# Kernel tuning notes

Hardware: AMD Instinct MI355X
Metric: run time of the kernel (lower is better)

The kernel has to match this reference:

```python
import jax, jax.numpy as jnp
import numpy as np

VOCAB, EMB, HID = 50257, 256, 512
B, S = 64, 512


def setup_inputs() -> dict:
    key = jax.random.key(0)
    ks = jax.random.split(key, 11)
    sc = 0.05
    return {
        "inputs": jax.random.randint(ks[0], (B, S), 0, VOCAB, dtype=jnp.int32),
        "emb": jax.random.normal(ks[1], (VOCAB, EMB), jnp.float32) * sc,
        "Wi": jax.random.normal(ks[2], (EMB, 4 * HID), jnp.float32) * sc,   # kernel, gate order i|f|g|o (Keras)
        "Wh": jax.random.normal(ks[3], (HID, 4 * HID), jnp.float32) * sc,   # recurrent kernel
        "b": jax.random.normal(ks[4], (4 * HID,), jnp.float32) * sc,
        "W1": jax.random.normal(ks[5], (HID, HID), jnp.float32) * sc,
        "b1": jnp.zeros((HID,), jnp.float32),
        "W2": jax.random.normal(ks[6], (HID, HID), jnp.float32) * sc,
        "b2": jnp.zeros((HID,), jnp.float32),
        "W3": jax.random.normal(ks[7], (HID, VOCAB), jnp.float32) * sc,
        "b3": jnp.zeros((VOCAB,), jnp.float32),
    }


def _lstm_final_h(x, Wi, Wh, b):
    # x: [B, S, E] -> final hidden state [B, H]
    Bsz = x.shape[0]
    H = Wh.shape[0]
    h0 = jnp.zeros((Bsz, H), x.dtype)
    c0 = jnp.zeros((Bsz, H), x.dtype)

    def step(carry, xt):
        h, c = carry
        z = xt @ Wi + h @ Wh + b              # [B, 4H]
        i, f, g, o = jnp.split(z, 4, axis=-1)  # Keras gate order: input, forget, cell, output
        i = jax.nn.sigmoid(i)
        f = jax.nn.sigmoid(f)
        g = jnp.tanh(g)
        o = jax.nn.sigmoid(o)
        c = f * c + i * g
        h = o * jnp.tanh(c)
        return (h, c), None

    (h, _), _ = jax.lax.scan(step, (h0, c0), jnp.swapaxes(x, 0, 1))  # scan over time [S, B, E]
    return h


def reference(inputs, emb, Wi, Wh, b, W1, b1, W2, b2, W3, b3):
    src_emb = emb[inputs]                      # [B, S, E] embedding lookup
    enc_hidden = _lstm_final_h(src_emb, Wi, Wh, b)  # [B, H]
    y = jnp.tanh(enc_hidden @ W1 + b1)
    y = jnp.tanh(y @ W2 + b2)
    logits = y @ W3 + b3                       # [B, vocab]
    return jax.nn.log_softmax(logits, axis=-1)
```

## Files before the change

### kernel.cpp

```cpp
#include <hip/hip_runtime.h>
#include <hip/hip_bf16.h>

#define VOCAB 50257
#define EMBD  256
#define HID   512
#define BATCH 64
#define SEQ   512

typedef short bf16x8 __attribute__((ext_vector_type(8)));
typedef float f32x4  __attribute__((ext_vector_type(4)));

__device__ inline short f2b(float f) {
    union { float f; unsigned u; } v; v.f = f;
    unsigned r = v.u + 0x7FFFu + ((v.u >> 16) & 1u);
    return (short)(r >> 16);
}
__device__ inline unsigned pack2_trunc(float lo, float hi) {
    union { float f; unsigned u; } a, b; a.f = lo; b.f = hi;
    return __builtin_amdgcn_perm(b.u, a.u, 0x07060302);
}
__device__ inline float fast_tanh(float x) {
    x = fminf(fmaxf(x, -15.f), 15.f);
    float e = __expf(2.f * x);
    return (e - 1.f) / (e + 1.f);
}
__device__ inline float fast_sig(float x) { return 1.f / (1.f + __expf(-x)); }

__device__ inline void load_x_frags(const float* __restrict__ emb, int idxv, int quad, bf16x8* Ax) {
#pragma unroll
    for (int kt = 0; kt < 8; ++kt) {
        const float* p = emb + (size_t)idxv * EMBD + kt * 32 + quad * 8;
        float4 e0 = *(const float4*)(p);
        float4 e1 = *(const float4*)(p + 4);
        union { bf16x8 v; unsigned u[4]; } f;
        f.u[0] = pack2_trunc(e0.x, e0.y);
        f.u[1] = pack2_trunc(e0.z, e0.w);
        f.u[2] = pack2_trunc(e1.x, e1.y);
        f.u[3] = pack2_trunc(e1.z, e1.w);
        Ax[kt] = f.v;
    }
}

__global__ __launch_bounds__(256, 1) void lstm_kernel(
    const int* __restrict__ idx, const float* __restrict__ emb,
    const float* __restrict__ Wi, const float* __restrict__ Wh,
    const float* __restrict__ bvec,
    unsigned long long* __restrict__ hbuf ,
    unsigned short* __restrict__ hfinal )
{
    const int wgid = blockIdx.x;
    const int grp  = wgid >> 5;
    const int jj   = wgid & 31;
    const int tid  = threadIdx.x;
    const int lane = tid & 63;
    const int w    = tid >> 6;
    const int quad = lane >> 4;
    const int l16  = lane & 15;
    const int cbase = jj * 16 + w * 4;
    const int wcol  = (l16 & 3) * HID + cbase + (l16 >> 2);
    const int arow  = grp * 16 + l16;

    __shared__ __align__(16) unsigned hstageF[2][4096];

    bf16x8 Bh[16], Bx[8];
#pragma unroll
    for (int kt = 0; kt < 16; ++kt)
#pragma unroll
        for (int i = 0; i < 8; ++i)
            Bh[kt][i] = f2b(Wh[(size_t)(kt * 32 + quad * 8 + i) * 2048 + wcol]);
#pragma unroll
    for (int kt = 0; kt < 8; ++kt)
#pragma unroll
        for (int i = 0; i < 8; ++i)
            Bx[kt][i] = f2b(Wi[(size_t)(kt * 32 + quad * 8 + i) * 2048 + wcol]);

    float bvr[4];
#pragma unroll
    for (int r = 0; r < 4; ++r) bvr[r] = bvec[r * HID + cbase + quad];

    bf16x8 Ax[8];
    load_x_frags(emb, idx[arow * SEQ], quad, Ax);

    const int scp = jj * 8 + w * 2 + (quad >> 1);
    const int su  = (scp >> 4) * 256 + ((scp >> 2) & 3) * 64 + l16 * 4 + (scp & 3);

    float cs = 0.f;

    for (int t = 0; t < SEQ; ++t) {
        const unsigned long long* rbase =
            hbuf + ((size_t)((t & 1) * 4 + grp) * 4096 + w * 1024 + lane);

        unsigned long long v[16];
        if (t > 0) {
#pragma unroll
            for (int i = 0; i < 16; ++i)
                v[i] = __hip_atomic_load(rbase + i * 64,
                                         __ATOMIC_RELAXED, __HIP_MEMORY_SCOPE_AGENT);
        }

        f32x4 a0 = {0.f, 0.f, 0.f, 0.f}, a1 = {0.f, 0.f, 0.f, 0.f};
#pragma unroll
        for (int kt = 0; kt < 8; kt += 2) {
            a0 = __builtin_amdgcn_mfma_f32_16x16x32_bf16(Bx[kt],     Ax[kt],     a0, 0, 0, 0);
            a1 = __builtin_amdgcn_mfma_f32_16x16x32_bf16(Bx[kt + 1], Ax[kt + 1], a1, 0, 0, 0);
        }

        if (t > 0) {
            const unsigned tg = (unsigned)t;
            while (true) {
                bool ok = true;
#pragma unroll
                for (int i = 0; i < 16; ++i)
                    ok = ok && ((unsigned)(v[i] >> 32) == tg);
                if (__ballot(ok) == ~0ull) break;
#pragma unroll
                for (int i = 0; i < 16; ++i)
                    v[i] = __hip_atomic_load(rbase + i * 64,
                                             __ATOMIC_RELAXED, __HIP_MEMORY_SCOPE_AGENT);
            }
#pragma unroll
            for (int i = 0; i < 16; ++i)
                hstageF[t & 1][w * 1024 + i * 64 + lane] = (unsigned)v[i];
        }
        __syncthreads();

        if (t > 0) {
            const unsigned* hp = &hstageF[t & 1][0];
#pragma unroll
            for (int kt = 0; kt < 16; kt += 2) {
                bf16x8 ha = *(const bf16x8*)(hp + kt * 256 + lane * 4);
                bf16x8 hb = *(const bf16x8*)(hp + (kt + 1) * 256 + lane * 4);
                a0 = __builtin_amdgcn_mfma_f32_16x16x32_bf16(Bh[kt],     ha, a0, 0, 0, 0);
                a1 = __builtin_amdgcn_mfma_f32_16x16x32_bf16(Bh[kt + 1], hb, a1, 0, 0, 0);
            }
        }

        float iG = fast_sig (a0[0] + a1[0] + bvr[0]);
        float fG = fast_sig (a0[1] + a1[1] + bvr[1]);
        float gG = fast_tanh(a0[2] + a1[2] + bvr[2]);
        float oG = fast_sig (a0[3] + a1[3] + bvr[3]);
        cs = fG * cs + iG * gG;
        float h  = oG * fast_tanh(cs);
        float hp2 = __shfl_xor(h, 16);
        unsigned pv = (unsigned)(unsigned short)f2b(h) |
                      ((unsigned)(unsigned short)f2b(hp2) << 16);

        if ((quad & 1) == 0) {
            unsigned long long val = (unsigned long long)pv |
                                     ((unsigned long long)(unsigned)(t + 1) << 32);
            unsigned long long* dst = hbuf +
                ((size_t)(((t + 1) & 1) * 4 + grp) * 4096 + su);
            __hip_atomic_store(dst, val, __ATOMIC_RELAXED, __HIP_MEMORY_SCOPE_AGENT);
            if (t == SEQ - 1)
                *(unsigned*)&hfinal[(size_t)(grp * 16 + l16) * HID + cbase + quad] = pv;
        }

        if (t + 1 < SEQ) {
            int nx = idx[arow * SEQ + t + 1];
            load_x_frags(emb, nx, quad, Ax);
        }
    }
}

__global__ __launch_bounds__(256, 1) void gemm_tanh_kernel(
    const unsigned short* __restrict__ A, const float* __restrict__ W,
    const float* __restrict__ bias, unsigned short* __restrict__ out)
{
    const int tid = threadIdx.x, lane = tid & 63, wave = tid >> 6;
    const int quad = lane >> 4, l16 = lane & 15;
    const int col = blockIdx.x * 16 + l16;
    bf16x8 Bw[16];
#pragma unroll
    for (int kt = 0; kt < 16; ++kt)
#pragma unroll
        for (int i = 0; i < 8; ++i)
            Bw[kt][i] = f2b(W[(size_t)(kt * 32 + quad * 8 + i) * HID + col]);
    f32x4 acc = {0.f, 0.f, 0.f, 0.f};
#pragma unroll
    for (int kt = 0; kt < 16; ++kt) {
        bf16x8 a = *(const bf16x8*)(A + (size_t)(wave * 16 + l16) * HID + kt * 32 + quad * 8);
        acc = __builtin_amdgcn_mfma_f32_16x16x32_bf16(a, Bw[kt], acc, 0, 0, 0);
    }
    const float bvv = bias[col];
#pragma unroll
    for (int r = 0; r < 4; ++r) {
        float y = fast_tanh(acc[r] + bvv);
        out[(size_t)(wave * 16 + quad * 4 + r) * HID + col] = (unsigned short)f2b(y);
    }
}

__global__ __launch_bounds__(256, 2) void logits_kernel(
    const unsigned short* __restrict__ A, const float* __restrict__ W3,
    const float* __restrict__ b3, float* __restrict__ outL)
{
    const int tid = threadIdx.x, lane = tid & 63, wave = tid >> 6;
    const int quad = lane >> 4, l16 = lane & 15;
    const int c0 = blockIdx.x * 64;
    const int col = c0 + wave * 16 + l16;
    const bool cok = col < VOCAB;
    const int colc = cok ? col : (VOCAB - 1);

    __shared__ unsigned short wt[256][68];

    f32x4 acc[4];
#pragma unroll
    for (int rt = 0; rt < 4; ++rt) acc[rt] = (f32x4){0.f, 0.f, 0.f, 0.f};

    const int kr = tid >> 4;
    const int cg = (tid & 15) * 4;

    for (int kc = 0; kc < 2; ++kc) {
#pragma unroll 4
        for (int it = 0; it < 16; ++it) {
            const int k = it * 16 + kr;
            const int gc = c0 + cg;
            float4 wv;
            if (gc + 3 < VOCAB) {
                wv = *(const float4*)&W3[(size_t)(kc * 256 + k) * VOCAB + gc];
            } else {
                const float* Wr = &W3[(size_t)(kc * 256 + k) * VOCAB];
                wv.x = (gc + 0 < VOCAB) ? Wr[gc + 0] : 0.f;
                wv.y = (gc + 1 < VOCAB) ? Wr[gc + 1] : 0.f;
                wv.z = (gc + 2 < VOCAB) ? Wr[gc + 2] : 0.f;
                wv.w = (gc + 3 < VOCAB) ? Wr[gc + 3] : 0.f;
            }
            unsigned short* d = &wt[k][cg];
            d[0] = (unsigned short)f2b(wv.x);
            d[1] = (unsigned short)f2b(wv.y);
            d[2] = (unsigned short)f2b(wv.z);
            d[3] = (unsigned short)f2b(wv.w);
        }
        __syncthreads();
        bf16x8 Bw[8];
#pragma unroll
        for (int kt = 0; kt < 8; ++kt)
#pragma unroll
            for (int i = 0; i < 8; ++i)
                Bw[kt][i] = (short)wt[kt * 32 + quad * 8 + i][wave * 16 + l16];
#pragma unroll
        for (int rt = 0; rt < 4; ++rt)
#pragma unroll
            for (int kt = 0; kt < 8; ++kt) {
                bf16x8 a = *(const bf16x8*)(A + (size_t)(rt * 16 + l16) * HID +
                                            kc * 256 + kt * 32 + quad * 8);
                acc[rt] = __builtin_amdgcn_mfma_f32_16x16x32_bf16(a, Bw[kt], acc[rt], 0, 0, 0);
            }
        __syncthreads();
    }
    const float bvv = b3[colc];
    if (cok) {
#pragma unroll
        for (int rt = 0; rt < 4; ++rt)
#pragma unroll
            for (int r = 0; r < 4; ++r)
                outL[(size_t)(rt * 16 + quad * 4 + r) * VOCAB + col] = acc[rt][r] + bvv;
    }
}

__global__ __launch_bounds__(256, 1) void lsm_kernel(
    const float* __restrict__ lg, float* __restrict__ out)
{
    const int row = blockIdx.x;
    const float* L = lg + (size_t)row * VOCAB;
    const float4* L4 = (const float4*)L;
    const int nv4 = VOCAB / 4;

    float m = -1e30f;
    for (int i = threadIdx.x; i < nv4; i += 256) {
        float4 v = L4[i];
        m = fmaxf(fmaxf(fmaxf(m, v.x), fmaxf(v.y, v.z)), v.w);
    }
    if (threadIdx.x == 0) m = fmaxf(m, L[VOCAB - 1]);
#pragma unroll
    for (int o = 32; o; o >>= 1) m = fmaxf(m, __shfl_xor(m, o));
    __shared__ float red[4], red2[4];
    if ((threadIdx.x & 63) == 0) red[threadIdx.x >> 6] = m;
    __syncthreads();
    m = fmaxf(fmaxf(red[0], red[1]), fmaxf(red[2], red[3]));

    float s = 0.f;
    for (int i = threadIdx.x; i < nv4; i += 256) {
        float4 v = L4[i];
        s += __expf(v.x - m) + __expf(v.y - m) + __expf(v.z - m) + __expf(v.w - m);
    }
    if (threadIdx.x == 0) s += __expf(L[VOCAB - 1] - m);
#pragma unroll
    for (int o = 32; o; o >>= 1) s += __shfl_xor(s, o);
    if ((threadIdx.x & 63) == 0) red2[threadIdx.x >> 6] = s;
    __syncthreads();
    s = red2[0] + red2[1] + red2[2] + red2[3];
    const float ls = m + __logf(s);

    float* O = out + (size_t)row * VOCAB;
    float4* O4 = (float4*)O;
    for (int i = threadIdx.x; i < nv4; i += 256) {
        float4 v = L4[i];
        O4[i] = (float4){v.x - ls, v.y - ls, v.z - ls, v.w - ls};
    }
    if (threadIdx.x == 0) O[VOCAB - 1] = L[VOCAB - 1] - ls;
}

extern "C" void kernel_launch(void* const* d_in, const int* in_sizes, int n_in,
                              void* d_out, int out_size, void* d_ws, size_t ws_size,
                              hipStream_t stream) {
    (void)in_sizes; (void)n_in; (void)out_size; (void)ws_size;
    const int*   idx = (const int*)d_in[0];
    const float* emb = (const float*)d_in[1];
    const float* Wi  = (const float*)d_in[2];
    const float* Wh  = (const float*)d_in[3];
    const float* b   = (const float*)d_in[4];
    const float* W1  = (const float*)d_in[5];
    const float* b1  = (const float*)d_in[6];
    const float* W2  = (const float*)d_in[7];
    const float* b2  = (const float*)d_in[8];
    const float* W3  = (const float*)d_in[9];
    const float* b3  = (const float*)d_in[10];
    float* out = (float*)d_out;

    char* w = (char*)d_ws;
    unsigned long long* hbuf   = (unsigned long long*)w;
    unsigned short*     y1     = (unsigned short*)w;
    unsigned short*     y2     = (unsigned short*)(w + 65536);
    unsigned short*     hfinal = (unsigned short*)(w + 262144);
    float*              logits = (float*)(w + 262144);

    lstm_kernel<<<128, 256, 0, stream>>>(idx, emb, Wi, Wh, b, hbuf, hfinal);
    gemm_tanh_kernel<<<HID / 16, 256, 0, stream>>>(hfinal, W1, b1, y1);
    gemm_tanh_kernel<<<HID / 16, 256, 0, stream>>>(y1, W2, b2, y2);
    logits_kernel<<<(VOCAB + 63) / 64, 256, 0, stream>>>(y2, W3, b3, logits);
    lsm_kernel<<<BATCH, 256, 0, stream>>>(logits, out);
}
```

Measured before the change: 2.218 ms.

## Poll a workgroup-scope mirror of hidden state with inline asm loads

Each LSTM step now writes the hidden state to a second mirror buffer with a workgroup-scope store as well as to the agent-scope buffer. Readers poll the mirror with raw global_load sc0 instructions, which may be served from a closer cache level, and fall back to agent-scope atomic loads after 32 failed rounds. The launch grows to 256 blocks, half of which exit at once, which changes the block-to-group mapping and probably how blocks land on XCDs so that cooperating blocks share an L2. The risk is relying on undefined cross-workgroup visibility, which could stall or read stale data; the timeout fallback exists to guard against that.

Result: no change. 2.241 ms (+1.1%).

```diff
diff --git a/kernel.cpp b/kernel.cpp
--- a/kernel.cpp
+++ b/kernel.cpp
@@ -41,16 +41,48 @@
     }
 }
 
-__global__ __launch_bounds__(256, 1) void lstm_kernel(
+__device__ inline void mirror_issue16(const unsigned long long* p, unsigned long long* v) {
+    asm volatile(
+        "global_load_dwordx2 %0,  %16, off sc0\n\t"
+        "global_load_dwordx2 %1,  %16, off offset:512 sc0\n\t"
+        "global_load_dwordx2 %2,  %16, off offset:1024 sc0\n\t"
+        "global_load_dwordx2 %3,  %16, off offset:1536 sc0\n\t"
+        "global_load_dwordx2 %4,  %17, off sc0\n\t"
+        "global_load_dwordx2 %5,  %17, off offset:512 sc0\n\t"
+        "global_load_dwordx2 %6,  %17, off offset:1024 sc0\n\t"
+        "global_load_dwordx2 %7,  %17, off offset:1536 sc0\n\t"
+        "global_load_dwordx2 %8,  %18, off sc0\n\t"
+        "global_load_dwordx2 %9,  %18, off offset:512 sc0\n\t"
+        "global_load_dwordx2 %10, %18, off offset:1024 sc0\n\t"
+        "global_load_dwordx2 %11, %18, off offset:1536 sc0\n\t"
+        "global_load_dwordx2 %12, %19, off sc0\n\t"
+        "global_load_dwordx2 %13, %19, off offset:512 sc0\n\t"
+        "global_load_dwordx2 %14, %19, off offset:1024 sc0\n\t"
+        "global_load_dwordx2 %15, %19, off offset:1536 sc0"
+        : "=&v"(v[0]), "=&v"(v[1]), "=&v"(v[2]), "=&v"(v[3]),
+          "=&v"(v[4]), "=&v"(v[5]), "=&v"(v[6]), "=&v"(v[7]),
+          "=&v"(v[8]), "=&v"(v[9]), "=&v"(v[10]), "=&v"(v[11]),
+          "=&v"(v[12]), "=&v"(v[13]), "=&v"(v[14]), "=&v"(v[15])
+        : "v"(p), "v"(p + 256), "v"(p + 512), "v"(p + 768)
+        : "memory");
+}
+__device__ inline void vm_fence() {
+    asm volatile("s_waitcnt vmcnt(0)" ::: "memory");
+    __builtin_amdgcn_sched_barrier(0);
+}
+
+__global__ __launch_bounds__(256, 2) void lstm_kernel(
     const int* __restrict__ idx, const float* __restrict__ emb,
     const float* __restrict__ Wi, const float* __restrict__ Wh,
     const float* __restrict__ bvec,
     unsigned long long* __restrict__ hbuf ,
+    unsigned long long* __restrict__ hmir ,
     unsigned short* __restrict__ hfinal )
 {
     const int wgid = blockIdx.x;
-    const int grp  = wgid >> 5;
-    const int jj   = wgid & 31;
+    if ((wgid & 7) >= 4) return;
+    const int grp  = wgid & 7;
+    const int jj   = wgid >> 3;
     const int tid  = threadIdx.x;
     const int lane = tid & 63;
     const int w    = tid >> 6;
@@ -85,17 +117,24 @@
     const int su  = (scp >> 4) * 256 + ((scp >> 2) & 3) * 64 + l16 * 4 + (scp & 3);
 
     float cs = 0.f;
+    bool mirSticky = true;
 
     for (int t = 0; t < SEQ; ++t) {
-        const unsigned long long* rbase =
-            hbuf + ((size_t)((t & 1) * 4 + grp) * 4096 + w * 1024 + lane);
+        const size_t off = (size_t)((t & 1) * 4 + grp) * 4096 + w * 1024 + lane;
+        const unsigned long long* rbM = hbuf + off;
+        const unsigned long long* rbL = hmir + off;
+        bool useMir = mirSticky;
 
         unsigned long long v[16];
         if (t > 0) {
-#pragma unroll
-            for (int i = 0; i < 16; ++i)
-                v[i] = __hip_atomic_load(rbase + i * 64,
-                                         __ATOMIC_RELAXED, __HIP_MEMORY_SCOPE_AGENT);
+            if (useMir) {
+                mirror_issue16(rbL, v);
+            } else {
+#pragma unroll
+                for (int i = 0; i < 16; ++i)
+                    v[i] = __hip_atomic_load(rbM + i * 64,
+                                             __ATOMIC_RELAXED, __HIP_MEMORY_SCOPE_AGENT);
+            }
         }
 
         f32x4 a0 = {0.f, 0.f, 0.f, 0.f}, a1 = {0.f, 0.f, 0.f, 0.f};
@@ -107,17 +146,25 @@
 
         if (t > 0) {
             const unsigned tg = (unsigned)t;
-            while (true) {
+            int rounds = 0;
+            for (;;) {
+                if (useMir) vm_fence();
                 bool ok = true;
 #pragma unroll
                 for (int i = 0; i < 16; ++i)
                     ok = ok && ((unsigned)(v[i] >> 32) == tg);
                 if (__ballot(ok) == ~0ull) break;
-#pragma unroll
-                for (int i = 0; i < 16; ++i)
-                    v[i] = __hip_atomic_load(rbase + i * 64,
-                                             __ATOMIC_RELAXED, __HIP_MEMORY_SCOPE_AGENT);
-            }
+                if (useMir && ++rounds >= 32) useMir = false;
+                if (useMir) {
+                    mirror_issue16(rbL, v);
+                } else {
+#pragma unroll
+                    for (int i = 0; i < 16; ++i)
+                        v[i] = __hip_atomic_load(rbM + i * 64,
+                                                 __ATOMIC_RELAXED, __HIP_MEMORY_SCOPE_AGENT);
+                }
+            }
+            if (!useMir && t >= 8) mirSticky = false;
 #pragma unroll
             for (int i = 0; i < 16; ++i)
                 hstageF[t & 1][w * 1024 + i * 64 + lane] = (unsigned)v[i];
@@ -148,9 +195,11 @@
         if ((quad & 1) == 0) {
             unsigned long long val = (unsigned long long)pv |
                                      ((unsigned long long)(unsigned)(t + 1) << 32);
-            unsigned long long* dst = hbuf +
-                ((size_t)(((t + 1) & 1) * 4 + grp) * 4096 + su);
-            __hip_atomic_store(dst, val, __ATOMIC_RELAXED, __HIP_MEMORY_SCOPE_AGENT);
+            const size_t soff = (size_t)(((t + 1) & 1) * 4 + grp) * 4096 + su;
+            __hip_atomic_store(hmir + soff, val, __ATOMIC_RELAXED,
+                               __HIP_MEMORY_SCOPE_WORKGROUP);
+            __hip_atomic_store(hbuf + soff, val, __ATOMIC_RELAXED,
+                               __HIP_MEMORY_SCOPE_AGENT);
             if (t == SEQ - 1)
                 *(unsigned*)&hfinal[(size_t)(grp * 16 + l16) * HID + cbase + quad] = pv;
         }
@@ -322,9 +371,10 @@
     unsigned short*     y1     = (unsigned short*)w;
     unsigned short*     y2     = (unsigned short*)(w + 65536);
     unsigned short*     hfinal = (unsigned short*)(w + 262144);
+    unsigned long long* hmir   = (unsigned long long*)(w + 327680);
     float*              logits = (float*)(w + 262144);
 
-    lstm_kernel<<<128, 256, 0, stream>>>(idx, emb, Wi, Wh, b, hbuf, hfinal);
+    lstm_kernel<<<256, 256, 0, stream>>>(idx, emb, Wi, Wh, b, hbuf, hmir, hfinal);
     gemm_tanh_kernel<<<HID / 16, 256, 0, stream>>>(hfinal, W1, b1, y1);
     gemm_tanh_kernel<<<HID / 16, 256, 0, stream>>>(y1, W2, b2, y2);
     logits_kernel<<<(VOCAB + 63) / 64, 256, 0, stream>>>(y2, W3, b3, logits);
```
